# Kernel tuning notes

Measured on AMD Instinct MI355X. Metric: run time of the kernel, lower is better.

Reference implementation:

```python
import jax, jax.numpy as jnp
import numpy as np

T, B, D, H = 2048, 32, 256, 256


def setup_inputs() -> dict:
    key = jax.random.key(0)
    ks = jax.random.split(key, 7)
    s = 1.0 / np.sqrt(H)
    return {
        "seq_embs": jax.random.normal(ks[0], (T, B, D), dtype=jnp.float32),
        "mask_x": jax.random.randint(ks[1], (T, B), 0, 2, dtype=jnp.int32),
        "hidden": jax.random.normal(ks[2], (B, H), dtype=jnp.float32),
        "w_ih": jax.random.uniform(ks[3], (3 * H, D), jnp.float32, -s, s),
        "w_hh": jax.random.uniform(ks[4], (3 * H, H), jnp.float32, -s, s),
        "b_ih": jax.random.uniform(ks[5], (3 * H,), jnp.float32, -s, s),
        "b_hh": jax.random.uniform(ks[6], (3 * H,), jnp.float32, -s, s),
    }


def reference(seq_embs, mask_x, hidden, w_ih, w_hh, b_ih, b_hh):
    # Precompute all input-side gate projections in one big GEMM: [T, B, 3H]
    gi_all = jnp.einsum("tbd,gd->tbg", seq_embs, w_ih) + b_ih
    mask_f = mask_x.astype(seq_embs.dtype)  # [T, B]

    def step(h, inp):
        gi, m_t = inp  # gi: [B, 3H], m_t: [B]
        gh = h @ w_hh.T + b_hh  # [B, 3H]
        i_r, i_z, i_n = jnp.split(gi, 3, axis=1)
        h_r, h_z, h_n = jnp.split(gh, 3, axis=1)
        r = jax.nn.sigmoid(i_r + h_r)
        z = jax.nn.sigmoid(i_z + h_z)
        n = jnp.tanh(i_n + r * h_n)
        h_t = (1.0 - z) * n + z * h  # GRUCell candidate hidden
        m = m_t[:, None]  # [B, 1]
        h_new = h_t * m + h * (1.0 - m)  # mask-gated state update
        return h_new, h_t * m  # output per step is masked candidate

    h_final, outputs = jax.lax.scan(step, hidden, (gi_all, mask_f))
    return outputs, h_final
```

## Files before the change

### kernel.cpp

```cpp
#include <hip/hip_runtime.h>
#include <hip/hip_bf16.h>

#define TT 2048
#define BB 32
#define DD 256
#define HH 256
#define GG 768

typedef _Float16 half2_t __attribute__((ext_vector_type(2)));
typedef _Float16 f16x8 __attribute__((ext_vector_type(8)));
typedef float    f32x4 __attribute__((ext_vector_type(4)));
typedef unsigned int u32x4 __attribute__((ext_vector_type(4)));

__device__ inline float ldgi(const float* p) { return *p; }
__device__ inline float ldgi(const __hip_bfloat16* p) { return __bfloat162float(*p); }
__device__ inline void stgi(float* p, float v) { *p = v; }
__device__ inline void stgi(__hip_bfloat16* p, float v) { *p = __float2bfloat16(v); }

__global__ __launch_bounds__(256)
void pack_w(const float* __restrict__ w, unsigned int* __restrict__ wf) {
    int idx = blockIdx.x * 256 + threadIdx.x;
    int r    = idx & 3;
    int l    = (idx >> 2) & 63;
    int kt   = (idx >> 8) & 7;
    int rest = idx >> 11;
    int nt = rest % 6, wv = rest / 6;
    int n = wv * 96 + nt * 16 + (l & 15);
    int k = kt * 32 + (l >> 4) * 8 + 2 * r;
    float a = w[(size_t)n * DD + k];
    float b = w[(size_t)n * DD + k + 1];
    half2_t h = {(_Float16)a, (_Float16)b};
    wf[idx] = __builtin_bit_cast(unsigned int, h);
}

template <typename GiT>
__global__ __launch_bounds__(256)
void gemm_gi_mfma(const float* __restrict__ A,
                  const float* __restrict__ W,
                  const float* __restrict__ bias,
                  GiT* __restrict__ C)
{
    __shared__ __align__(16) _Float16 Asl[128][40];
    __shared__ __align__(16) _Float16 Bsl[128][40];

    const int tid = threadIdx.x;
    const int wv  = tid >> 6;
    const int l   = tid & 63;
    const int wm  = (wv & 1) * 64;
    const int wn  = (wv >> 1) * 64;
    const size_t bm = (size_t)blockIdx.y * 128;
    const int    bn = blockIdx.x * 128;

    const int lr = tid >> 3;
    const int lc = (tid & 7) * 4;

    f32x4 acc[4][4] = {};

    for (int kt = 0; kt < 256; kt += 32) {
#pragma unroll
        for (int rr = 0; rr < 128; rr += 32) {
            float4 av = *(const float4*)&A[(bm + lr + rr) * DD + kt + lc];
            half2_t p0 = {(_Float16)av.x, (_Float16)av.y};
            half2_t p1 = {(_Float16)av.z, (_Float16)av.w};
            uint2 pk = {__builtin_bit_cast(unsigned int, p0),
                        __builtin_bit_cast(unsigned int, p1)};
            *(uint2*)&Asl[lr + rr][lc] = pk;
        }
#pragma unroll
        for (int rr = 0; rr < 128; rr += 32) {
            float4 bv = *(const float4*)&W[(size_t)(bn + lr + rr) * DD + kt + lc];
            half2_t p0 = {(_Float16)bv.x, (_Float16)bv.y};
            half2_t p1 = {(_Float16)bv.z, (_Float16)bv.w};
            uint2 pk = {__builtin_bit_cast(unsigned int, p0),
                        __builtin_bit_cast(unsigned int, p1)};
            *(uint2*)&Bsl[lr + rr][lc] = pk;
        }
        __syncthreads();

        f16x8 af[4], bf[4];
#pragma unroll
        for (int i = 0; i < 4; ++i) {
            af[i] = *(const f16x8*)&Asl[wm + i * 16 + (l & 15)][(l >> 4) * 8];
            bf[i] = *(const f16x8*)&Bsl[wn + i * 16 + (l & 15)][(l >> 4) * 8];
        }
#pragma unroll
        for (int mi = 0; mi < 4; ++mi)
#pragma unroll
            for (int ni = 0; ni < 4; ++ni)
                acc[mi][ni] = __builtin_amdgcn_mfma_f32_16x16x32_f16(
                    af[mi], bf[ni], acc[mi][ni], 0, 0, 0);
        __syncthreads();
    }

    const int crow = (l >> 4) * 4;
    const int ccol = l & 15;
#pragma unroll
    for (int ni = 0; ni < 4; ++ni) {
        int n = bn + wn + ni * 16 + ccol;
        float bs = bias[n];
#pragma unroll
        for (int mi = 0; mi < 4; ++mi) {
#pragma unroll
            for (int q = 0; q < 4; ++q) {
                size_t m = bm + wm + mi * 16 + crow + q;
                stgi(&C[m * GG + n], acc[mi][ni][q] + bs);
            }
        }
    }
}

template <typename GiT>
__global__ void
__attribute__((amdgpu_flat_work_group_size(512, 512), amdgpu_waves_per_eu(2, 2)))
gru_scan_mfma(const GiT* __restrict__ gi,
              const int* __restrict__ mask,
              const float* __restrict__ h0,
              const unsigned int* __restrict__ wf,
              const float* __restrict__ b_hh,
              float* __restrict__ out,
              float* __restrict__ hfin)
{
    const int b   = blockIdx.x;
    const int tid = threadIdx.x;
    const int wv  = tid >> 6;
    const int l   = tid & 63;

    __shared__ __align__(16) _Float16 hhalf[HH];
    __shared__ float gh_lds[GG];
    __shared__ int mlds[TT];

    u32x4 w[6][8];
    {
        const u32x4* wp = (const u32x4*)wf;
#pragma unroll
        for (int nt = 0; nt < 6; ++nt)
#pragma unroll
            for (int kt = 0; kt < 8; ++kt)
                w[nt][kt] = wp[(size_t)((wv * 6 + nt) * 8 + kt) * 64 + l];
    }
#pragma unroll
    for (int nt = 0; nt < 6; ++nt)
#pragma unroll
        for (int kt = 0; kt < 8; ++kt)
            asm volatile("" : "+a"(w[nt][kt]));

    for (int i = tid; i < TT; i += 512)
        mlds[i] = mask[i * BB + b];

    float h_r = 0.f, bh0 = 0.f, bh1 = 0.f, bh2 = 0.f;
    if (tid < HH) {
        h_r = h0[b * HH + tid];
        hhalf[tid] = (_Float16)h_r;
        bh0 = b_hh[tid];
        bh1 = b_hh[tid + HH];
        bh2 = b_hh[tid + 2 * HH];
    }
    __syncthreads();

    const _Float16* abase = hhalf + (l >> 4) * 8;

    for (int ts = 0; ts < TT; ++ts) {
        if (mlds[ts]) {
            float ir = 0.f, iz = 0.f, inn = 0.f;
            if (tid < HH) {
                const GiT* gtb = gi + ((size_t)ts * BB + b) * GG;
                ir  = ldgi(gtb + tid);
                iz  = ldgi(gtb + tid + HH);
                inn = ldgi(gtb + tid + 2 * HH);
            }

            f32x4 acc[6] = {};
#pragma unroll
            for (int kt = 0; kt < 8; ++kt) {
                f16x8 a = *(const f16x8*)(abase + kt * 32);
#pragma unroll
                for (int nt = 0; nt < 6; ++nt)
                    acc[nt] = __builtin_amdgcn_mfma_f32_16x16x32_f16(
                        a, __builtin_bit_cast(f16x8, w[nt][kt]), acc[nt],
                        0, 0, 0);
            }
            if (l < 16) {
#pragma unroll
                for (int nt = 0; nt < 6; ++nt)
                    gh_lds[wv * 96 + nt * 16 + l] = acc[nt][0];
            }
            __syncthreads();

            if (tid < HH) {
                float hr = gh_lds[tid] + bh0;
                float hz = gh_lds[tid + HH] + bh1;
                float hn = gh_lds[tid + 2 * HH] + bh2;
                float r = 1.f / (1.f + __expf(-(ir + hr)));
                float z = 1.f / (1.f + __expf(-(iz + hz)));
                float e = __expf(2.f * (inn + r * hn));
                float n = 1.f - 2.f / (e + 1.f);
                float ht = (1.f - z) * n + z * h_r;
                out[((size_t)ts * BB + b) * HH + tid] = ht;
                h_r = ht;
                hhalf[tid] = (_Float16)ht;
            }
            __syncthreads();
        } else {
            if (tid < HH)
                out[((size_t)ts * BB + b) * HH + tid] = 0.f;
        }
    }
    if (tid < HH) hfin[b * HH + tid] = h_r;
}

extern "C" void kernel_launch(void* const* d_in, const int* in_sizes, int n_in,
                              void* d_out, int out_size, void* d_ws, size_t ws_size,
                              hipStream_t stream) {
    const float* seq  = (const float*)d_in[0];
    const int*   mask = (const int*)  d_in[1];
    const float* h0   = (const float*)d_in[2];
    const float* w_ih = (const float*)d_in[3];
    const float* w_hh = (const float*)d_in[4];
    const float* b_ih = (const float*)d_in[5];
    const float* b_hh = (const float*)d_in[6];

    float* out  = (float*)d_out;
    float* hfin = out + (size_t)TT * BB * HH;

    const size_t wf_elems = (size_t)128 * GG;
    unsigned int* wf = (unsigned int*)d_ws;
    const size_t gi_elems = (size_t)TT * BB * GG;
    const size_t need_f32 = wf_elems * 4 + gi_elems * 4;

    pack_w<<<(int)(wf_elems / 256), 256, 0, stream>>>(w_hh, wf);

    dim3 ggrid(GG / 128, (TT * BB) / 128);
    if (ws_size >= need_f32) {
        float* gip = (float*)d_ws + wf_elems;
        gemm_gi_mfma<float><<<ggrid, 256, 0, stream>>>(seq, w_ih, b_ih, gip);
        gru_scan_mfma<float><<<BB, 512, 0, stream>>>(gip, mask, h0, wf, b_hh,
                                                     out, hfin);
    } else {
        __hip_bfloat16* gip = (__hip_bfloat16*)((float*)d_ws + wf_elems);
        gemm_gi_mfma<__hip_bfloat16><<<ggrid, 256, 0, stream>>>(seq, w_ih, b_ih, gip);
        gru_scan_mfma<__hip_bfloat16><<<BB, 512, 0, stream>>>(gip, mask, h0, wf,
                                                              b_hh, out, hfin);
    }
}
```

Before: 1.500 ms.

## Move recurrent weights from registers to LDS plus per-step global streaming

Recurrent W_hh fragments were previously held in AGPRs for the whole scan. They are now split: the first three K-tiles live in LDS, and the remaining five are reloaded from global memory (expected to hit in L2) every active timestep. The mask is also compressed into a 64-bit bitmask in LDS. This frees a large register budget, but it adds LDS reads and global weight loads to the latency-critical serial recurrence on every step.

```diff
diff --git a/kernel.cpp b/kernel.cpp
--- a/kernel.cpp
+++ b/kernel.cpp
@@ -7,6 +7,9 @@
 #define HH 256
 #define GG 768
 
+#define KT_LDS 3
+#define KT_STR 5
+
 typedef _Float16 half2_t __attribute__((ext_vector_type(2)));
 typedef _Float16 f16x8 __attribute__((ext_vector_type(8)));
 typedef float    f32x4 __attribute__((ext_vector_type(4)));
@@ -19,18 +22,19 @@
 
 __global__ __launch_bounds__(256)
 void pack_w(const float* __restrict__ w, unsigned int* __restrict__ wf) {
-    int idx = blockIdx.x * 256 + threadIdx.x;
-    int r    = idx & 3;
-    int l    = (idx >> 2) & 63;
-    int kt   = (idx >> 8) & 7;
-    int rest = idx >> 11;
-    int nt = rest % 6, wv = rest / 6;
+    int i = blockIdx.x * 256 + threadIdx.x;
+    int r   = i & 3;
+    int l   = (i >> 2) & 63;
+    int e   = i >> 8;
+    int nt6 = e % 48;
+    int kt  = e / 48;
+    int wv  = nt6 / 6, nt = nt6 % 6;
     int n = wv * 96 + nt * 16 + (l & 15);
     int k = kt * 32 + (l >> 4) * 8 + 2 * r;
     float a = w[(size_t)n * DD + k];
     float b = w[(size_t)n * DD + k + 1];
     half2_t h = {(_Float16)a, (_Float16)b};
-    wf[idx] = __builtin_bit_cast(unsigned int, h);
+    wf[i] = __builtin_bit_cast(unsigned int, h);
 }
 
 template <typename GiT>
@@ -125,27 +129,22 @@
     const int wv  = tid >> 6;
     const int l   = tid & 63;
 
+    __shared__ u32x4 wlds[KT_LDS * 48 * 64];
     __shared__ __align__(16) _Float16 hhalf[HH];
     __shared__ float gh_lds[GG];
-    __shared__ int mlds[TT];
-
-    u32x4 w[6][8];
-    {
-        const u32x4* wp = (const u32x4*)wf;
-#pragma unroll
-        for (int nt = 0; nt < 6; ++nt)
-#pragma unroll
-            for (int kt = 0; kt < 8; ++kt)
-                w[nt][kt] = wp[(size_t)((wv * 6 + nt) * 8 + kt) * 64 + l];
-    }
-#pragma unroll
-    for (int nt = 0; nt < 6; ++nt)
-#pragma unroll
-        for (int kt = 0; kt < 8; ++kt)
-            asm volatile("" : "+a"(w[nt][kt]));
-
-    for (int i = tid; i < TT; i += 512)
-        mlds[i] = mask[i * BB + b];
+    __shared__ unsigned long long mbits[TT / 64];
+
+    const u32x4* wp4 = (const u32x4*)wf;
+
+    for (int i = tid; i < KT_LDS * 48 * 64; i += 512)
+        wlds[i] = wp4[i];
+
+    if (tid < TT / 64) {
+        unsigned long long v = 0;
+        for (int s = 0; s < 64; ++s)
+            v |= (mask[(tid * 64 + s) * BB + b] ? 1ull : 0ull) << s;
+        mbits[tid] = v;
+    }
 
     float h_r = 0.f, bh0 = 0.f, bh1 = 0.f, bh2 = 0.f;
     if (tid < HH) {
@@ -158,9 +157,18 @@
     __syncthreads();
 
     const _Float16* abase = hhalf + (l >> 4) * 8;
+    const u32x4* wstr  = wp4 + (size_t)(KT_LDS * 48 + wv * 6) * 64 + l;
+    const u32x4* wldsb = wlds + (size_t)(wv * 6) * 64 + l;
 
     for (int ts = 0; ts < TT; ++ts) {
-        if (mlds[ts]) {
+        if ((mbits[ts >> 6] >> (ts & 63)) & 1ull) {
+            u32x4 ws[KT_STR][6];
+#pragma unroll
+            for (int s = 0; s < KT_STR; ++s)
+#pragma unroll
+                for (int nt = 0; nt < 6; ++nt)
+                    ws[s][nt] = wstr[(size_t)(s * 48 + nt) * 64];
+
             float ir = 0.f, iz = 0.f, inn = 0.f;
             if (tid < HH) {
                 const GiT* gtb = gi + ((size_t)ts * BB + b) * GG;
@@ -171,12 +179,22 @@
 
             f32x4 acc[6] = {};
 #pragma unroll
-            for (int kt = 0; kt < 8; ++kt) {
+            for (int kt = 0; kt < KT_LDS; ++kt) {
                 f16x8 a = *(const f16x8*)(abase + kt * 32);
+#pragma unroll
+                for (int nt = 0; nt < 6; ++nt) {
+                    u32x4 wv4 = wldsb[(size_t)(kt * 48 + nt) * 64];
+                    acc[nt] = __builtin_amdgcn_mfma_f32_16x16x32_f16(
+                        a, __builtin_bit_cast(f16x8, wv4), acc[nt], 0, 0, 0);
+                }
+            }
+#pragma unroll
+            for (int s = 0; s < KT_STR; ++s) {
+                f16x8 a = *(const f16x8*)(abase + (KT_LDS + s) * 32);
 #pragma unroll
                 for (int nt = 0; nt < 6; ++nt)
                     acc[nt] = __builtin_amdgcn_mfma_f32_16x16x32_f16(
-                        a, __builtin_bit_cast(f16x8, w[nt][kt]), acc[nt],
+                        a, __builtin_bit_cast(f16x8, ws[s][nt]), acc[nt],
                         0, 0, 0);
             }
             if (l < 16) {
```

After: 2.811 ms. 87.4% more time.
